# Kernel optimization log

Hardware: AMD Instinct MI355X
Metric: run time of the kernel (lower is better)

The kernel has to match this reference:

```python
import jax, jax.numpy as jnp
import numpy as np

K0 = 16                       # probe slice length (hard-coded in kernel)
TAU = 2.053748910631823       # t-test threshold (|tau| of kernel constant)


def setup_inputs() -> dict:
    key = jax.random.key(0)
    k1, k2, k3 = jax.random.split(key, 3)
    B, DIN, DOUT = 8192, 4096, 4096
    x = jax.random.normal(k1, (B, DIN), dtype=jnp.float32)
    W = jax.random.normal(k2, (DOUT, DIN), dtype=jnp.float32)
    bias = jax.random.normal(k3, (DOUT,), dtype=jnp.float32)
    return {"x": x, "W": W, "bias": bias}


def reference(x, W, bias):
    # --- partial dot over the first K0 columns of K (the probe) ---
    x0 = x[:, :K0]                    # [B, K0]
    w0 = W[:, :K0]                    # [DOUT, K0]
    y1 = x0 @ w0.T                    # [B, DOUT]  sum_k x_k * w_k
    # sum of squared elementwise products: prod_k^2 = x_k^2 * w_k^2
    s2 = (x0 * x0) @ (w0 * w0).T      # [B, DOUT]
    # --- per-(row, column) t-statistic and early-exit decision ---
    tstat = jnp.abs(y1) / jnp.sqrt(s2 / K0)
    passed = tstat < TAU              # True -> column deemed insignificant, zeroed
    # --- full linear (active columns keep full accumulation + bias) ---
    full = x @ W.T + bias[None, :]    # [B, DOUT]
    return jnp.where(passed, 0.0, full)
```

## Files before the change

kernel.cpp:

```cpp
#include <hip/hip_runtime.h>
#include <cstdint>
#include <cstddef>

#define TAU_D 2.053748910631823
#define M_DIM 8192
#define N_DIM 4096
#define K_DIM 4096
#define NIT   32

typedef float f32x4  __attribute__((ext_vector_type(4)));
typedef short bf16x8 __attribute__((ext_vector_type(8)));

typedef __attribute__((address_space(1))) void gvoid_t;
typedef __attribute__((address_space(3))) void lvoid_t;

__device__ __forceinline__ void gload_lds16(const void* g, void* l) {
    __builtin_amdgcn_global_load_lds((const gvoid_t*)g, (lvoid_t*)l, 16, 0, 0);
}

__device__ __forceinline__ unsigned int pack2bf(float lo, float hi) {
    unsigned int ul = __float_as_uint(lo);
    unsigned int uh = __float_as_uint(hi);
    ul = (ul + 0x7FFFu + ((ul >> 16) & 1u)) >> 16;
    uh = (uh + 0x7FFFu + ((uh >> 16) & 1u)) >> 16;
    return ul | (uh << 16);
}

__global__ void cvt_f32_to_bf16(const float4* __restrict__ in,
                                uint2* __restrict__ out, int n4) {
    int i = blockIdx.x * blockDim.x + threadIdx.x;
    const int stride = gridDim.x * blockDim.x;
    for (; i < n4; i += stride) {
        float4 a = in[i];
        uint2 o;
        o.x = pack2bf(a.x, a.y);
        o.y = pack2bf(a.z, a.w);
        out[i] = o;
    }
}

#define BAR() do { __builtin_amdgcn_s_barrier(); \
                   asm volatile("" ::: "memory"); } while (0)

__global__ __launch_bounds__(512, 2) void gemm_masked8(
    const unsigned short* __restrict__ Ab,
    const unsigned short* __restrict__ Bb,
    const float* __restrict__ X,
    const float* __restrict__ Wt,
    const float* __restrict__ bias,
    float* __restrict__ out)
{
    __shared__ __align__(16) char lds[131072];

    const int tid  = threadIdx.x;
    const int wave = tid >> 6;
    const int lane = tid & 63;
    const int lr = lane & 15;
    const int lq = lane >> 4;
    const int wm = wave >> 2;
    const int wn = wave & 3;

    const int flat = blockIdx.x;
    const int xcd  = flat & 7;
    const int s    = flat >> 3;
    const int rnd  = s >> 5;
    const int jj   = s & 31;
    const int trow = rnd * 16 + ((xcd >> 2) << 3) + (jj >> 2);
    const int tcol = ((xcd & 3) << 2) + (jj & 3);
    const int rowBase = trow * 256;
    const int colBase = tcol * 256;

    f32x4 acc[8][4];
    #pragma unroll
    for (int i = 0; i < 8; ++i)
        #pragma unroll
        for (int n = 0; n < 4; ++n)
            acc[i][n] = (f32x4){0.f, 0.f, 0.f, 0.f};

    const int srow  = tid >> 3;
    const int sslot = (tid & 7) ^ (srow & 7);
    const unsigned short* aSrc =
        Ab + (size_t)(rowBase + srow) * K_DIM + sslot * 8;
    const unsigned short* bSrc =
        Bb + (size_t)(colBase + srow) * K_DIM + sslot * 8;

    const unsigned R0A = 0, R0B = 32768, R1A = 65536, R1B = 98304;

    auto stageHalfA = [&](int kst, unsigned reg, int h) {
        #pragma unroll
        for (int i = 2 * h; i < 2 * h + 2; ++i)
            gload_lds16(aSrc + (size_t)i * 64 * K_DIM + kst * 64,
                        lds + reg + i * 8192 + wave * 1024);
    };
    auto stageHalfB = [&](int kst, unsigned reg, int h) {
        #pragma unroll
        for (int i = 2 * h; i < 2 * h + 2; ++i)
            gload_lds16(bSrc + (size_t)i * 64 * K_DIM + kst * 64,
                        lds + reg + i * 8192 + wave * 1024);
    };

    const unsigned kk0 = (unsigned)((lq) ^ (lr & 7)) * 16;
    const unsigned kk1 = (unsigned)((4 + lq) ^ (lr & 7)) * 16;
    const unsigned rowA = (unsigned)(wm * 128 + lr) * 128;
    const unsigned rowB = (unsigned)(wn * 64 + lr) * 128;

    bf16x8 A0[4][2];
    bf16x8 A1[4][2];
    bf16x8 B0R0[2][2];
    bf16x8 B0R1[2][2];
    bf16x8 B1[2][2];

    stageHalfA(0, R0A, 0); stageHalfA(0, R0A, 1);
    stageHalfB(0, R0B, 0); stageHalfB(0, R0B, 1);
    stageHalfB(1, R1B, 0); stageHalfB(1, R1B, 1);
    asm volatile("s_waitcnt vmcnt(4)" ::: "memory");
    __builtin_amdgcn_s_barrier();
    asm volatile("" ::: "memory");
    #pragma unroll
    for (int m = 0; m < 4; ++m) {
        A0[m][0] = *(const bf16x8*)(lds + R0A + rowA + m * 2048 + kk0);
        A0[m][1] = *(const bf16x8*)(lds + R0A + rowA + m * 2048 + kk1);
    }
    #pragma unroll
    for (int n = 0; n < 2; ++n) {
        B0R0[n][0] = *(const bf16x8*)(lds + R0B + rowB + n * 2048 + kk0);
        B0R0[n][1] = *(const bf16x8*)(lds + R0B + rowB + n * 2048 + kk1);
    }

    #define MFMA_QUAD(ACC_M, ACC_N, AREG, BREG)                                \
        do {                                                                   \
            __builtin_amdgcn_s_setprio(1);                                     \
            _Pragma("unroll")                                                  \
            for (int m = 0; m < 4; ++m)                                        \
                _Pragma("unroll")                                              \
                for (int n = 0; n < 2; ++n)                                    \
                    _Pragma("unroll")                                          \
                    for (int ks = 0; ks < 2; ++ks)                             \
                        acc[(ACC_M) + m][(ACC_N) + n] =                        \
                            __builtin_amdgcn_mfma_f32_16x16x32_bf16(           \
                                AREG[m][ks], BREG[n][ks],                      \
                                acc[(ACC_M) + m][(ACC_N) + n], 0, 0, 0);       \
            __builtin_amdgcn_s_setprio(0);                                     \
        } while (0)

    for (int j = 0; j < NIT; ++j) {
        const int ka = 2 * j;
        const int kb = 2 * j + 1;
        const bool stg = (j + 1 < NIT);

        BAR();
        #pragma unroll
        for (int n = 0; n < 2; ++n) {
            B1[n][0] = *(const bf16x8*)(lds + R0B + rowB + (2 + n) * 2048 + kk0);
            B1[n][1] = *(const bf16x8*)(lds + R0B + rowB + (2 + n) * 2048 + kk1);
        }
        stageHalfA(kb, R1A, 0);
        MFMA_QUAD(0, 0, A0, B0R0);

        BAR();
        #pragma unroll
        for (int m = 0; m < 4; ++m) {
            A1[m][0] = *(const bf16x8*)(lds + R0A + rowA + (4 + m) * 2048 + kk0);
            A1[m][1] = *(const bf16x8*)(lds + R0A + rowA + (4 + m) * 2048 + kk1);
        }
        stageHalfA(kb, R1A, 1);
        MFMA_QUAD(0, 2, A0, B1);

        BAR();
        if (stg) stageHalfB(ka + 2, R0B, 0);
        MFMA_QUAD(4, 2, A1, B1);
        if (stg) asm volatile("s_waitcnt vmcnt(2)" ::: "memory");
        else     asm volatile("s_waitcnt vmcnt(0)" ::: "memory");

        BAR();
        #pragma unroll
        for (int m = 0; m < 4; ++m) {
            A0[m][0] = *(const bf16x8*)(lds + R1A + rowA + m * 2048 + kk0);
            A0[m][1] = *(const bf16x8*)(lds + R1A + rowA + m * 2048 + kk1);
        }
        #pragma unroll
        for (int n = 0; n < 2; ++n) {
            B0R1[n][0] = *(const bf16x8*)(lds + R1B + rowB + n * 2048 + kk0);
            B0R1[n][1] = *(const bf16x8*)(lds + R1B + rowB + n * 2048 + kk1);
        }
        if (stg) stageHalfB(ka + 2, R0B, 1);
        MFMA_QUAD(4, 0, A1, B0R0);

        BAR();
        #pragma unroll
        for (int n = 0; n < 2; ++n) {
            B1[n][0] = *(const bf16x8*)(lds + R1B + rowB + (2 + n) * 2048 + kk0);
            B1[n][1] = *(const bf16x8*)(lds + R1B + rowB + (2 + n) * 2048 + kk1);
        }
        if (stg) stageHalfA(ka + 2, R0A, 0);
        MFMA_QUAD(0, 0, A0, B0R1);

        BAR();
        #pragma unroll
        for (int m = 0; m < 4; ++m) {
            A1[m][0] = *(const bf16x8*)(lds + R1A + rowA + (4 + m) * 2048 + kk0);
            A1[m][1] = *(const bf16x8*)(lds + R1A + rowA + (4 + m) * 2048 + kk1);
        }
        if (stg) stageHalfA(ka + 2, R0A, 1);
        MFMA_QUAD(0, 2, A0, B1);

        BAR();
        if (stg) stageHalfB(kb + 2, R1B, 0);
        MFMA_QUAD(4, 2, A1, B1);
        if (stg) asm volatile("s_waitcnt vmcnt(2)" ::: "memory");
        else     asm volatile("s_waitcnt vmcnt(0)" ::: "memory");

        BAR();
        if (stg) {
            #pragma unroll
            for (int m = 0; m < 4; ++m) {
                A0[m][0] = *(const bf16x8*)(lds + R0A + rowA + m * 2048 + kk0);
                A0[m][1] = *(const bf16x8*)(lds + R0A + rowA + m * 2048 + kk1);
            }
            #pragma unroll
            for (int n = 0; n < 2; ++n) {
                B0R0[n][0] = *(const bf16x8*)(lds + R0B + rowB + n * 2048 + kk0);
                B0R0[n][1] = *(const bf16x8*)(lds + R0B + rowB + n * 2048 + kk1);
            }
            stageHalfB(kb + 2, R1B, 1);
        }
        MFMA_QUAD(4, 0, A1, B0R1);
    }

    __syncthreads();
    float* x0s = (float*)(lds);
    float* w0s = (float*)(lds + 16384);
    #pragma unroll
    for (int i = 0; i < 2; ++i) {
        int idx = tid + i * 512;
        int r = idx >> 2, qq = (idx & 3) << 2;
        *(f32x4*)(x0s + r * 16 + qq) =
            *(const f32x4*)(X + (size_t)(rowBase + r) * K_DIM + qq);
        *(f32x4*)(w0s + r * 16 + qq) =
            *(const f32x4*)(Wt + (size_t)(colBase + r) * K_DIM + qq);
    }
    __syncthreads();

    const float TAU32 = (float)TAU_D;

    #pragma unroll
    for (int np = 0; np < 4; np += 2) {
        float wv[2][16];
        float bv[2];
        #pragma unroll
        for (int e = 0; e < 2; ++e) {
            const int c = wn * 64 + (np + e) * 16 + lr;
            #pragma unroll
            for (int q = 0; q < 4; ++q)
                *(f32x4*)&wv[e][q * 4] = *(const f32x4*)(w0s + c * 16 + q * 4);
            bv[e] = bias[colBase + c];
        }
        #pragma unroll
        for (int mi = 0; mi < 8; ++mi) {
            #pragma unroll
            for (int jr = 0; jr < 4; ++jr) {
                const int rw = wm * 128 + mi * 16 + lq * 4 + jr;
                float xv[16];
                #pragma unroll
                for (int q = 0; q < 4; ++q)
                    *(f32x4*)&xv[q * 4] = *(const f32x4*)(x0s + rw * 16 + q * 4);
                const size_t orow = (size_t)(rowBase + rw) * N_DIM + colBase;
                #pragma unroll
                for (int e = 0; e < 2; ++e) {
                    const int n = np + e;
                    float y1 = 0.f, s2 = 0.f;
                    #pragma unroll
                    for (int k = 0; k < 16; ++k) {
                        float xk = xv[k], wk = wv[e][k];
                        float xx = xk * xk, ww = wk * wk;
                        y1 = fmaf(xk, wk, y1);
                        s2 = fmaf(xx, ww, s2);
                    }
                    float t = fabsf(y1) / sqrtf(s2 * 0.0625f);
                    float v = (t < TAU32) ? 0.0f : (acc[mi][n][jr] + bv[e]);
                    out[orow + wn * 64 + n * 16 + lr] = v;
                }
            }
        }
    }
}

__global__ __launch_bounds__(256, 2) void gemm_masked_fb(
    const float* __restrict__ X, const float* __restrict__ Wt,
    const float* __restrict__ bias, float* __restrict__ out)
{
    __shared__ __align__(16) unsigned short As[128 * 32];
    __shared__ __align__(16) unsigned short Bs[128 * 32];

    const int tid  = threadIdx.x;
    const int wave = tid >> 6;
    const int lane = tid & 63;
    const int rowBase = blockIdx.y * 128;
    const int colBase = blockIdx.x * 128;
    const int wr = wave >> 1;
    const int wc = wave & 1;
    const int lr = lane & 15;
    const int lq = lane >> 4;

    f32x4 acc[4][4];
    #pragma unroll
    for (int m = 0; m < 4; ++m)
        #pragma unroll
        for (int n = 0; n < 4; ++n)
            acc[m][n] = (f32x4){0.f, 0.f, 0.f, 0.f};

    const int srow = tid >> 2;
    const int scol = (tid & 3) * 8;
    const float* afp = X  + (size_t)(rowBase + srow) * K_DIM + scol;
    const float* bfp = Wt + (size_t)(colBase + srow) * K_DIM + scol;

    for (int kt = 0; kt < K_DIM; kt += 32) {
        #pragma unroll
        for (int issue = 0; issue < 2; ++issue) {
            const float* sa = afp + (size_t)issue * 64 * K_DIM;
            const float* sb = bfp + (size_t)issue * 64 * K_DIM;
            float4 a0 = *(const float4*)(sa);
            float4 a1 = *(const float4*)(sa + 4);
            float4 b0 = *(const float4*)(sb);
            float4 b1 = *(const float4*)(sb + 4);
            uint4 pa, pb;
            pa.x = pack2bf(a0.x, a0.y); pa.y = pack2bf(a0.z, a0.w);
            pa.z = pack2bf(a1.x, a1.y); pa.w = pack2bf(a1.z, a1.w);
            pb.x = pack2bf(b0.x, b0.y); pb.y = pack2bf(b0.z, b0.w);
            pb.z = pack2bf(b1.x, b1.y); pb.w = pack2bf(b1.z, b1.w);
            *(uint4*)((char*)As + issue * 4096 + tid * 16) = pa;
            *(uint4*)((char*)Bs + issue * 4096 + tid * 16) = pb;
        }
        afp += 32; bfp += 32;
        __syncthreads();

        bf16x8 af[4], bq[4];
        #pragma unroll
        for (int m = 0; m < 4; ++m)
            af[m] = *(const bf16x8*)(As + (wr * 64 + m * 16 + lr) * 32 + lq * 8);
        #pragma unroll
        for (int n = 0; n < 4; ++n)
            bq[n] = *(const bf16x8*)(Bs + (wc * 64 + n * 16 + lr) * 32 + lq * 8);
        #pragma unroll
        for (int m = 0; m < 4; ++m)
            #pragma unroll
            for (int n = 0; n < 4; ++n)
                acc[m][n] = __builtin_amdgcn_mfma_f32_16x16x32_bf16(
                    af[m], bq[n], acc[m][n], 0, 0, 0);
        __syncthreads();
    }

    float* x0s = (float*)As;
    float* w0s = (float*)Bs;
    #pragma unroll
    for (int i = 0; i < 2; ++i) {
        int idx = tid + i * 256;
        int r = idx >> 2, q = (idx & 3) * 4;
        *(float4*)(x0s + r * 16 + q) =
            *(const float4*)(X + (size_t)(rowBase + r) * K_DIM + q);
        *(float4*)(w0s + r * 16 + q) =
            *(const float4*)(Wt + (size_t)(colBase + r) * K_DIM + q);
    }
    __syncthreads();

    const float TAU32 = (float)TAU_D;
    float wv[4][16];
    float bv[4];
    #pragma unroll
    for (int n = 0; n < 4; ++n) {
        int c = wc * 64 + n * 16 + lr;
        #pragma unroll
        for (int q = 0; q < 4; ++q)
            *(f32x4*)&wv[n][q * 4] = *(const f32x4*)(w0s + c * 16 + q * 4);
        bv[n] = bias[colBase + c];
    }

    #pragma unroll
    for (int m = 0; m < 4; ++m) {
        #pragma unroll
        for (int j = 0; j < 4; ++j) {
            const int r = wr * 64 + m * 16 + lq * 4 + j;
            float xv[16];
            #pragma unroll
            for (int q = 0; q < 4; ++q)
                *(f32x4*)&xv[q * 4] = *(const f32x4*)(x0s + r * 16 + q * 4);
            const size_t orow = (size_t)(rowBase + r) * N_DIM + colBase;
            #pragma unroll
            for (int n = 0; n < 4; ++n) {
                float y1 = 0.f, s2 = 0.f;
                #pragma unroll
                for (int k = 0; k < 16; ++k) {
                    float xk = xv[k];
                    float wk = wv[n][k];
                    float xx = xk * xk;
                    float ww = wk * wk;
                    y1 = fmaf(xk, wk, y1);
                    s2 = fmaf(xx, ww, s2);
                }
                float t = fabsf(y1) / sqrtf(s2 * 0.0625f);
                float v = (t < TAU32) ? 0.0f : (acc[m][n][j] + bv[n]);
                out[orow + wc * 64 + n * 16 + lr] = v;
            }
        }
    }
}

extern "C" void kernel_launch(void* const* d_in, const int* in_sizes, int n_in,
                              void* d_out, int out_size, void* d_ws, size_t ws_size,
                              hipStream_t stream) {
    const float* x    = (const float*)d_in[0];
    const float* W    = (const float*)d_in[1];
    const float* bias = (const float*)d_in[2];
    float* out = (float*)d_out;

    const size_t needA = (size_t)M_DIM * K_DIM * 2;
    const size_t needB = (size_t)N_DIM * K_DIM * 2;

    if (ws_size >= needA + needB) {
        unsigned short* xb = (unsigned short*)d_ws;
        unsigned short* wb = (unsigned short*)((char*)d_ws + needA);
        cvt_f32_to_bf16<<<2048, 256, 0, stream>>>(
            (const float4*)x, (uint2*)xb, (M_DIM * K_DIM) / 4);
        cvt_f32_to_bf16<<<2048, 256, 0, stream>>>(
            (const float4*)W, (uint2*)wb, (N_DIM * K_DIM) / 4);
        dim3 grid((M_DIM / 256) * (N_DIM / 256));
        gemm_masked8<<<grid, 512, 0, stream>>>(xb, wb, x, W, bias, out);
    } else {
        dim3 grid(N_DIM / 128, M_DIM / 128);
        gemm_masked_fb<<<grid, 256, 0, stream>>>(x, W, bias, out);
    }
}
```

Baseline: 323.3 us.

## Collapse double-buffered MFMA register fragments into single A/B fragment sets

Replaces the A0/A1/B0R0/B0R1/B1 fragment arrays with one A fragment set and two B fragment sets. Each phase now reloads its fragments from LDS right before its MFMA quad instead of prefetching them a phase ahead. The prologue barrier and initial fragment preload are removed, and the vmcnt waits are moved and loosened to match the new staging order. The aim is to lower VGPR pressure. The cost is that LDS read latency is exposed directly before the MFMAs rather than hidden behind the previous quad.

Measured after the change: 312.1 us. -3.5%, faster.

```diff
diff --git a/kernel.cpp b/kernel.cpp
--- a/kernel.cpp
+++ b/kernel.cpp
@@ -104,30 +104,16 @@
     const unsigned rowA = (unsigned)(wm * 128 + lr) * 128;
     const unsigned rowB = (unsigned)(wn * 64 + lr) * 128;
 
-    bf16x8 A0[4][2];
-    bf16x8 A1[4][2];
-    bf16x8 B0R0[2][2];
-    bf16x8 B0R1[2][2];
-    bf16x8 B1[2][2];
-
     stageHalfA(0, R0A, 0); stageHalfA(0, R0A, 1);
     stageHalfB(0, R0B, 0); stageHalfB(0, R0B, 1);
     stageHalfB(1, R1B, 0); stageHalfB(1, R1B, 1);
     asm volatile("s_waitcnt vmcnt(4)" ::: "memory");
-    __builtin_amdgcn_s_barrier();
-    asm volatile("" ::: "memory");
-    #pragma unroll
-    for (int m = 0; m < 4; ++m) {
-        A0[m][0] = *(const bf16x8*)(lds + R0A + rowA + m * 2048 + kk0);
-        A0[m][1] = *(const bf16x8*)(lds + R0A + rowA + m * 2048 + kk1);
-    }
-    #pragma unroll
-    for (int n = 0; n < 2; ++n) {
-        B0R0[n][0] = *(const bf16x8*)(lds + R0B + rowB + n * 2048 + kk0);
-        B0R0[n][1] = *(const bf16x8*)(lds + R0B + rowB + n * 2048 + kk1);
-    }
-
-    #define MFMA_QUAD(ACC_M, ACC_N, AREG, BREG)                                \
+
+    bf16x8 aF[4][2];
+    bf16x8 bF0[2][2];
+    bf16x8 bF1[2][2];
+
+    #define MFMA_QUAD(ACC_M, ACC_N, BREG)                                      \
         do {                                                                   \
             __builtin_amdgcn_s_setprio(1);                                     \
             _Pragma("unroll")                                                  \
@@ -138,7 +124,7 @@
                     for (int ks = 0; ks < 2; ++ks)                             \
                         acc[(ACC_M) + m][(ACC_N) + n] =                        \
                             __builtin_amdgcn_mfma_f32_16x16x32_bf16(           \
-                                AREG[m][ks], BREG[n][ks],                      \
+                                aF[m][ks], BREG[n][ks],                        \
                                 acc[(ACC_M) + m][(ACC_N) + n], 0, 0, 0);       \
             __builtin_amdgcn_s_setprio(0);                                     \
         } while (0)
@@ -150,81 +136,78 @@
 
         BAR();
         #pragma unroll
+        for (int m = 0; m < 4; ++m) {
+            aF[m][0] = *(const bf16x8*)(lds + R0A + rowA + m * 2048 + kk0);
+            aF[m][1] = *(const bf16x8*)(lds + R0A + rowA + m * 2048 + kk1);
+        }
+        #pragma unroll
         for (int n = 0; n < 2; ++n) {
-            B1[n][0] = *(const bf16x8*)(lds + R0B + rowB + (2 + n) * 2048 + kk0);
-            B1[n][1] = *(const bf16x8*)(lds + R0B + rowB + (2 + n) * 2048 + kk1);
+            bF0[n][0] = *(const bf16x8*)(lds + R0B + rowB + n * 2048 + kk0);
+            bF0[n][1] = *(const bf16x8*)(lds + R0B + rowB + n * 2048 + kk1);
         }
         stageHalfA(kb, R1A, 0);
-        MFMA_QUAD(0, 0, A0, B0R0);
+        MFMA_QUAD(0, 0, bF0);
+
+        BAR();
+        #pragma unroll
+        for (int n = 0; n < 2; ++n) {
+            bF1[n][0] = *(const bf16x8*)(lds + R0B + rowB + (2 + n) * 2048 + kk0);
+            bF1[n][1] = *(const bf16x8*)(lds + R0B + rowB + (2 + n) * 2048 + kk1);
+        }
+        stageHalfA(kb, R1A, 1);
+        MFMA_QUAD(0, 2, bF1);
 
         BAR();
         #pragma unroll
         for (int m = 0; m < 4; ++m) {
-            A1[m][0] = *(const bf16x8*)(lds + R0A + rowA + (4 + m) * 2048 + kk0);
-            A1[m][1] = *(const bf16x8*)(lds + R0A + rowA + (4 + m) * 2048 + kk1);
-        }
-        stageHalfA(kb, R1A, 1);
-        MFMA_QUAD(0, 2, A0, B1);
-
-        BAR();
+            aF[m][0] = *(const bf16x8*)(lds + R0A + rowA + (4 + m) * 2048 + kk0);
+            aF[m][1] = *(const bf16x8*)(lds + R0A + rowA + (4 + m) * 2048 + kk1);
+        }
         if (stg) stageHalfB(ka + 2, R0B, 0);
-        MFMA_QUAD(4, 2, A1, B1);
-        if (stg) asm volatile("s_waitcnt vmcnt(2)" ::: "memory");
+        MFMA_QUAD(4, 2, bF1);
+
+        BAR();
+        if (stg) stageHalfB(ka + 2, R0B, 1);
+        MFMA_QUAD(4, 0, bF0);
+        if (stg) asm volatile("s_waitcnt vmcnt(4)" ::: "memory");
         else     asm volatile("s_waitcnt vmcnt(0)" ::: "memory");
 
         BAR();
         #pragma unroll
         for (int m = 0; m < 4; ++m) {
-            A0[m][0] = *(const bf16x8*)(lds + R1A + rowA + m * 2048 + kk0);
-            A0[m][1] = *(const bf16x8*)(lds + R1A + rowA + m * 2048 + kk1);
+            aF[m][0] = *(const bf16x8*)(lds + R1A + rowA + m * 2048 + kk0);
+            aF[m][1] = *(const bf16x8*)(lds + R1A + rowA + m * 2048 + kk1);
         }
         #pragma unroll
         for (int n = 0; n < 2; ++n) {
-            B0R1[n][0] = *(const bf16x8*)(lds + R1B + rowB + n * 2048 + kk0);
-            B0R1[n][1] = *(const bf16x8*)(lds + R1B + rowB + n * 2048 + kk1);
-        }
-        if (stg) stageHalfB(ka + 2, R0B, 1);
-        MFMA_QUAD(4, 0, A1, B0R0);
+            bF0[n][0] = *(const bf16x8*)(lds + R1B + rowB + n * 2048 + kk0);
+            bF0[n][1] = *(const bf16x8*)(lds + R1B + rowB + n * 2048 + kk1);
+        }
+        if (stg) stageHalfA(ka + 2, R0A, 0);
+        MFMA_QUAD(0, 0, bF0);
 
         BAR();
         #pragma unroll
         for (int n = 0; n < 2; ++n) {
-            B1[n][0] = *(const bf16x8*)(lds + R1B + rowB + (2 + n) * 2048 + kk0);
-            B1[n][1] = *(const bf16x8*)(lds + R1B + rowB + (2 + n) * 2048 + kk1);
-        }
-        if (stg) stageHalfA(ka + 2, R0A, 0);
-        MFMA_QUAD(0, 0, A0, B0R1);
+            bF1[n][0] = *(const bf16x8*)(lds + R1B + rowB + (2 + n) * 2048 + kk0);
+            bF1[n][1] = *(const bf16x8*)(lds + R1B + rowB + (2 + n) * 2048 + kk1);
+        }
+        if (stg) stageHalfA(ka + 2, R0A, 1);
+        MFMA_QUAD(0, 2, bF1);
 
         BAR();
         #pragma unroll
         for (int m = 0; m < 4; ++m) {
-            A1[m][0] = *(const bf16x8*)(lds + R1A + rowA + (4 + m) * 2048 + kk0);
-            A1[m][1] = *(const bf16x8*)(lds + R1A + rowA + (4 + m) * 2048 + kk1);
-        }
-        if (stg) stageHalfA(ka + 2, R0A, 1);
-        MFMA_QUAD(0, 2, A0, B1);
-
-        BAR();
+            aF[m][0] = *(const bf16x8*)(lds + R1A + rowA + (4 + m) * 2048 + kk0);
+            aF[m][1] = *(const bf16x8*)(lds + R1A + rowA + (4 + m) * 2048 + kk1);
+        }
         if (stg) stageHalfB(kb + 2, R1B, 0);
-        MFMA_QUAD(4, 2, A1, B1);
-        if (stg) asm volatile("s_waitcnt vmcnt(2)" ::: "memory");
-        else     asm volatile("s_waitcnt vmcnt(0)" ::: "memory");
-
-        BAR();
-        if (stg) {
-            #pragma unroll
-            for (int m = 0; m < 4; ++m) {
-                A0[m][0] = *(const bf16x8*)(lds + R0A + rowA + m * 2048 + kk0);
-                A0[m][1] = *(const bf16x8*)(lds + R0A + rowA + m * 2048 + kk1);
-            }
-            #pragma unroll
-            for (int n = 0; n < 2; ++n) {
-                B0R0[n][0] = *(const bf16x8*)(lds + R0B + rowB + n * 2048 + kk0);
-                B0R0[n][1] = *(const bf16x8*)(lds + R0B + rowB + n * 2048 + kk1);
-            }
-            stageHalfB(kb + 2, R1B, 1);
-        }
-        MFMA_QUAD(4, 0, A1, B0R1);
+        MFMA_QUAD(4, 2, bF1);
+
+        BAR();
+        if (stg) stageHalfB(kb + 2, R1B, 1);
+        MFMA_QUAD(4, 0, bF0);
+        if (stg) asm volatile("s_waitcnt vmcnt(4)" ::: "memory");
     }
 
     __syncthreads();
```
